# Kernel optimization log

Hardware: AMD Instinct MI355X
Metric: run time of the kernel (lower is better)

The kernel has to match this reference:

```python
import jax, jax.numpy as jnp
import numpy as np

# dims matching init_kwargs
B = 4096
NFIELD = 20
NFEAT = 100000
SQL_NEMB = 16
DATA_NEMB = 16
HID = 512
K = 16          # num_experts
C = 2           # select_experts (top-k)
OUT = 1
CARD = NFIELD + NFEAT + 1  # sql embedding rows
GATE_IN = NFIELD * SQL_NEMB   # 320
EXP_IN = NFIELD * DATA_NEMB   # 320
EPS = 1e-10


def _xavier(key, shape):
    fan_in, fan_out = shape[-2], shape[-1]
    a = np.sqrt(6.0 / (fan_in + fan_out)).astype(np.float32)
    return jax.random.uniform(key, shape, jnp.float32, -a, a)


def setup_inputs() -> dict:
    key = jax.random.key(0)
    ks = jax.random.split(key, 12)
    x = jax.random.randint(ks[0], (B, NFIELD), 0, NFEAT, dtype=jnp.int64)
    sql = jax.random.randint(ks[1], (B, NFIELD), 0, CARD, dtype=jnp.int64)
    return {
        "x": x,
        "sql": sql,
        "sql_emb_w": _xavier(ks[2], (CARD, SQL_NEMB)),
        "inp_emb_w": _xavier(ks[3], (NFEAT, DATA_NEMB)),
        # gate network: Linear(GATE_IN->HID) + relu + Linear(HID->K) + softmax
        "gw1": _xavier(ks[4], (GATE_IN, HID)),
        "gb1": jnp.zeros((HID,), jnp.float32),
        "gw2": _xavier(ks[5], (HID, K)),
        "gb2": jnp.zeros((K,), jnp.float32),
        # K expert DNNs: Linear(EXP_IN->HID) + relu + Linear(HID->OUT)
        "ew1": _xavier(ks[6], (K, EXP_IN, HID)),
        "eb1": jnp.zeros((K, HID), jnp.float32),
        "ew2": _xavier(ks[7], (K, HID, OUT)),
        "eb2": jnp.zeros((K, OUT), jnp.float32),
    }


def _cv_squared(v):
    # coefficient-of-variation squared, Shazeer-style load-balancing term
    return jnp.var(v) / (jnp.mean(v) ** 2 + EPS)


def reference(x, sql, sql_emb_w, inp_emb_w, gw1, gb1, gw2, gb2, ew1, eb1, ew2, eb2):
    b = x.shape[0]
    x_emb = inp_emb_w[x].reshape(b, -1)      # [B, NFIELD*DATA_NEMB]
    sql_emb = sql_emb_w[sql].reshape(b, -1)  # [B, NFIELD*SQL_NEMB]

    # gate network -> softmax scores over K experts
    h = jax.nn.relu(sql_emb @ gw1 + gb1)
    gate_scores = jax.nn.softmax(h @ gw2 + gb2, axis=-1)  # [B, K]

    # top-C sparse gating: keep top-C scores, renormalize, zero the rest
    top_v, top_i = jax.lax.top_k(gate_scores, C)
    top_v = top_v / jnp.sum(top_v, axis=-1, keepdims=True)
    gates = jnp.zeros((b, K), gate_scores.dtype).at[jnp.arange(b)[:, None], top_i].set(top_v)

    # expert MLPs (batched over expert dim; zero gates nullify unselected experts)
    eh = jax.nn.relu(jnp.einsum('bi,kih->bkh', x_emb, ew1) + eb1)   # [B, K, HID]
    eo = jnp.einsum('bkh,kho->bko', eh, ew2) + eb2                   # [B, K, OUT]
    y = jnp.sum(gates[:, :, None] * eo, axis=1).squeeze(-1)          # [B]

    importance = jnp.sum(gates, axis=0)                              # [K]
    load = jnp.sum((gates > 0).astype(gates.dtype), axis=0)         # [K]
    loss = _cv_squared(importance) + _cv_squared(load)
    return y, loss
```

## Files before the change

kernel.cpp:

```cpp
#include <hip/hip_runtime.h>

#define Bn 4096
#define NF 20
#define NEMB 16
#define HIDN 512
#define KE 16
#define GIN 320
#define NKS 10

typedef __attribute__((ext_vector_type(8))) short short8;
typedef __attribute__((ext_vector_type(4))) float f32x4;

__device__ __forceinline__ unsigned short f2bf(float f) {
  unsigned int u = __builtin_bit_cast(unsigned int, f);
  u += 0x7fff + ((u >> 16) & 1);
  return (unsigned short)(u >> 16);
}
__device__ __forceinline__ float bf2f(unsigned short h) {
  unsigned int u = ((unsigned int)h) << 16;
  return __builtin_bit_cast(float, u);
}

__device__ __forceinline__ void gload_lds16(const unsigned short* g, void* l) {
  __builtin_amdgcn_global_load_lds(
      (const __attribute__((address_space(1))) unsigned int*)g,
      (__attribute__((address_space(3))) unsigned int*)l, 16, 0, 0);
}

__device__ __forceinline__ void vwait(int n) {
  if (n >= 5) asm volatile("s_waitcnt vmcnt(5)" ::: "memory");
  else        asm volatile("s_waitcnt vmcnt(0)" ::: "memory");
  __builtin_amdgcn_sched_barrier(0);
}

__global__ __launch_bounds__(256) void prep_kernel(
    const int* __restrict__ sql, const float* __restrict__ semb,
    const float* __restrict__ gw1, const float* __restrict__ ew1,
    unsigned short* __restrict__ SH, unsigned short* __restrict__ SL,
    unsigned short* __restrict__ GWF, unsigned short* __restrict__ EWF,
    float* __restrict__ y, int* __restrict__ cnt) {
  long long t = (long long)blockIdx.x * 256 + threadIdx.x;
  if (t < 81920) {
    int row = (int)(t / NF), f = (int)(t % NF);
    int idx = sql[row * NF + f];
    const float4* s = (const float4*)(semb + (size_t)idx * NEMB);
    float4 v[4] = {s[0], s[1], s[2], s[3]};
    const float* sf = (const float*)v;
    short8 h0, h1, l0, l1;
#pragma unroll
    for (int i = 0; i < 8; i++) {
      float a = sf[i];
      unsigned short hb = f2bf(a);
      h0[i] = (short)hb; l0[i] = (short)f2bf(a - bf2f(hb));
      a = sf[8 + i];
      hb = f2bf(a);
      h1[i] = (short)hb; l1[i] = (short)f2bf(a - bf2f(hb));
    }
    size_t o = (size_t)row * GIN + f * NEMB;
    *(short8*)(SH + o) = h0; *(short8*)(SH + o + 8) = h1;
    *(short8*)(SL + o) = l0; *(short8*)(SL + o + 8) = l1;
    return;
  }
  t -= 81920;
  if (t < 40960) {
    int s = (int)(t / 20480), r = (int)(t % 20480);
    int ks = r / 2048, r2 = r % 2048, nt = r2 / 64, l = r2 % 64;
    int k0 = ks * 32 + (l >> 4) * 8, n = nt * 16 + (l & 15);
    short8 o;
#pragma unroll
    for (int j = 0; j < 8; j++) {
      float w = gw1[(size_t)(k0 + j) * HIDN + n];
      unsigned short hb = f2bf(w);
      o[j] = (s == 0) ? (short)hb : (short)f2bf(w - bf2f(hb));
    }
    *(short8*)(GWF + ((((size_t)s * NKS + ks) * 32 + nt) * 64 + l) * 8) = o;
    return;
  }
  t -= 40960;
  if (t < 327680) {
    int e = (int)(t / 20480), r = (int)(t % 20480);
    int ks = r / 2048, r2 = r % 2048, nt = r2 / 64, l = r2 % 64;
    int k0 = ks * 32 + (l >> 4) * 8, n = nt * 16 + (l & 15);
    const float* W = ew1 + (size_t)e * GIN * HIDN;
    short8 o;
#pragma unroll
    for (int j = 0; j < 8; j++) o[j] = (short)f2bf(W[(size_t)(k0 + j) * HIDN + n]);
    *(short8*)(EWF + ((((size_t)e * NKS + ks) * 32 + nt) * 64 + l) * 8) = o;
    return;
  }
  t -= 327680;
  if (t < Bn + 1) y[t] = 0.f;
  else if (t < Bn + 1 + KE) cnt[t - (Bn + 1)] = 0;
}

__global__ __launch_bounds__(256, 2) void gate_kernel(
    const unsigned short* __restrict__ SH, const unsigned short* __restrict__ SL,
    const unsigned short* __restrict__ GWF, const float* __restrict__ gb1,
    const float* __restrict__ gw2, float* __restrict__ glp) {
  __shared__ __align__(16) unsigned short ring[3][10240];
  __shared__ float hs[64][68];
  const int tid = threadIdx.x, lane = tid & 63, wv = tid >> 6;
  const int bid = blockIdx.x;
  const int xcd = bid & 7, r_ = bid >> 3;
  const int cb = r_ & 7;
  const int band = (8 * xcd + (r_ >> 3)) * 64;
  const int ntg = cb * 4 + wv;

  short8 bh[NKS], bl[NKS];
#pragma unroll
  for (int ks = 0; ks < NKS; ks++) {
    bh[ks] = *(const short8*)(GWF + ((size_t)(ks * 32 + ntg)) * 512 + lane * 8);
    bl[ks] = *(const short8*)(GWF + ((size_t)((NKS + ks) * 32 + ntg)) * 512 + lane * 8);
  }
  const int cl = wv * 16 + (lane & 15);
  const float b1v = gb1[cb * 64 + cl];
  __builtin_amdgcn_sched_barrier(0);

#define GSTG(pi, slot)                                                        \
  {                                                                           \
    _Pragma("unroll") for (int i = 0; i < 5; i++) {                           \
      int c = wv * 5 + i;                                                     \
      int hl = c >= 10, kss = c - hl * 10;                                    \
      const unsigned short* s_ = (hl ? SL : SH) +                             \
          (size_t)(band + (pi) * 16 + (lane & 15)) * GIN + kss * 32 +         \
          (lane >> 4) * 8;                                                    \
      gload_lds16(s_, &ring[slot][c * 512 + lane * 8]);                       \
    }                                                                         \
  }

  GSTG(0, 0) GSTG(1, 1)
  __builtin_amdgcn_sched_barrier(0);

#pragma unroll
  for (int p = 0; p < 4; p++) {
    vwait(p < 3 ? 5 : 0);
    __builtin_amdgcn_s_barrier();
    __builtin_amdgcn_sched_barrier(0);
    if (p + 2 < 4) GSTG(p + 2, (p + 2) % 3)
    __builtin_amdgcn_sched_barrier(0);
    const unsigned short* rb = ring[p % 3];
    f32x4 acc = {};
#pragma unroll
    for (int ks = 0; ks < NKS; ks++) {
      short8 ah = *(const short8*)&rb[ks * 512 + lane * 8];
      short8 al = *(const short8*)&rb[(NKS + ks) * 512 + lane * 8];
      acc = __builtin_amdgcn_mfma_f32_16x16x32_bf16(ah, bh[ks], acc, 0, 0, 0);
      acc = __builtin_amdgcn_mfma_f32_16x16x32_bf16(al, bh[ks], acc, 0, 0, 0);
      acc = __builtin_amdgcn_mfma_f32_16x16x32_bf16(ah, bl[ks], acc, 0, 0, 0);
    }
#pragma unroll
    for (int j = 0; j < 4; j++)
      hs[p * 16 + (lane >> 4) * 4 + j][cl] = fmaxf(acc[j] + b1v, 0.f);
  }
  __syncthreads();

  float (*g2s)[16] = (float(*)[16])&ring[0][0];
  ((float4*)g2s)[tid] = ((const float4*)(gw2 + (size_t)cb * 64 * KE))[tid];
  __syncthreads();
#pragma unroll
  for (int it = 0; it < 4; it++) {
    int row = it * 16 + (tid >> 4), q = tid & 15;
    float s = 0.f;
#pragma unroll 8
    for (int c = 0; c < 64; c++) s = fmaf(hs[row][c], g2s[c][q], s);
    glp[((size_t)cb * Bn + band + row) * KE + q] = s;
  }
#undef GSTG
}

__global__ __launch_bounds__(256) void gate2_kernel(
    const float* __restrict__ glp, const float* __restrict__ gb2,
    int* __restrict__ cnt, int* __restrict__ list, float* __restrict__ wlist) {
  __shared__ float part[4][64][KE];
  __shared__ int lcnt[KE];
  __shared__ int gbase[KE];
  const int tid = threadIdx.x;
  const int r = tid & 63, g = tid >> 6;
  const int row = blockIdx.x * 64 + r;
  if (tid < KE) lcnt[tid] = 0;
  float lg[KE];
#pragma unroll
  for (int q = 0; q < KE; q++) lg[q] = 0.f;
#pragma unroll
  for (int s2 = 0; s2 < 2; s2++) {
    const float4* a = (const float4*)(glp + ((size_t)(2 * g + s2) * Bn + row) * KE);
#pragma unroll
    for (int u = 0; u < 4; u++) {
      float4 v = a[u];
      lg[u * 4 + 0] += v.x; lg[u * 4 + 1] += v.y;
      lg[u * 4 + 2] += v.z; lg[u * 4 + 3] += v.w;
    }
  }
#pragma unroll
  for (int q = 0; q < KE; q++) part[g][r][q] = lg[q];
  __syncthreads();
  if (tid < 64) {
#pragma unroll
    for (int q = 0; q < KE; q++)
      lg[q] = part[0][tid][q] + part[1][tid][q] + part[2][tid][q] +
              part[3][tid][q] + gb2[q];
    float m = lg[0];
#pragma unroll
    for (int q = 1; q < KE; q++) m = fmaxf(m, lg[q]);
    float e[KE];
#pragma unroll
    for (int q = 0; q < KE; q++) e[q] = expf(lg[q] - m);
    int i1 = 0; float v1 = e[0];
#pragma unroll
    for (int q = 1; q < KE; q++) if (e[q] > v1) { v1 = e[q]; i1 = q; }
    int i2 = (i1 == 0) ? 1 : 0; float v2 = e[i2];
#pragma unroll
    for (int q = 0; q < KE; q++)
      if (q != i1 && e[q] > v2) { v2 = e[q]; i2 = q; }
    int rowg = blockIdx.x * 64 + tid;
    int o1 = atomicAdd(&lcnt[i1], 1);
    int o2 = atomicAdd(&lcnt[i2], 1);
    __syncthreads();
    if (tid < KE) gbase[tid] = atomicAdd(&cnt[tid], lcnt[tid]);
    __syncthreads();
    float den = v1 + v2;
    int s1 = gbase[i1] + o1;
    list[i1 * Bn + s1] = rowg; wlist[i1 * Bn + s1] = v1 / den;
    int s2 = gbase[i2] + o2;
    list[i2 * Bn + s2] = rowg; wlist[i2 * Bn + s2] = v2 / den;
  } else {
    __syncthreads();
    __syncthreads();
  }
}

__global__ __launch_bounds__(256) void packloss_kernel(
    const int* __restrict__ x, const float* __restrict__ demb,
    const int* __restrict__ cnt, const int* __restrict__ list,
    const float* __restrict__ wlist, unsigned short* __restrict__ XEP,
    float* __restrict__ out) {
  __shared__ float simp[KE][KE];
  __shared__ float fimp[KE];
  const int tid = threadIdx.x;
  const int bid = blockIdx.x;
  const int xcd = bid & 7, r_ = bid >> 3;
  const int k = xcd + 8 * (r_ & 1), jb = r_ >> 1;
  if (jb == 64) {
    if (k != 0) return;
    const int kk = tid >> 4, g = tid & 15;
    const int n = cnt[kk];
    float s = 0.f;
    for (int j = g; j < n; j += 16) s += wlist[kk * Bn + j];
    simp[kk][g] = s;
    __syncthreads();
    if (tid < KE) {
      float t = 0.f;
      for (int q = 0; q < KE; q++) t += simp[tid][q];
      fimp[tid] = t;
    }
    __syncthreads();
    if (tid == 0) {
      double mi = 0.0, ml = 0.0;
      for (int q = 0; q < KE; q++) { mi += fimp[q]; ml += (double)cnt[q]; }
      mi /= KE; ml /= KE;
      double vi = 0.0, vl = 0.0;
      for (int q = 0; q < KE; q++) {
        double di = fimp[q] - mi; vi += di * di;
        double dl = (double)cnt[q] - ml; vl += dl * dl;
      }
      vi /= KE; vl /= KE;
      out[Bn] = (float)(vi / (mi * mi + 1e-10) + vl / (ml * ml + 1e-10));
    }
    return;
  }
  const int n = cnt[k];
  if (jb * 64 >= n) return;
  unsigned short* reg = XEP + (size_t)k * 1310720;
#pragma unroll
  for (int it = 0; it < 5; it++) {
    int tt = it * 256 + tid;
    int i = jb * 64 + tt / NF, f = tt % NF;
    if (i < n) {
      int rid = list[k * Bn + i];
      int idx = x[rid * NF + f];
      const float4* s = (const float4*)(demb + (size_t)idx * NEMB);
      float4 v[4] = {s[0], s[1], s[2], s[3]};
      const float* sf = (const float*)v;
      short8 o0, o1;
#pragma unroll
      for (int e = 0; e < 8; e++) {
        o0[e] = (short)f2bf(sf[e]);
        o1[e] = (short)f2bf(sf[8 + e]);
      }
      int panel = i >> 5, mt = (i >> 4) & 1, lr = i & 15;
      int ks = f >> 1, ko0 = (f & 1) * 2;
      unsigned short* d =
          reg + (size_t)panel * 10240 + ks * 1024 + mt * 512 + ko0 * 128 + lr * 8;
      *(short8*)d = o0;
      *(short8*)(d + 128) = o1;
    }
  }
}

__global__ __launch_bounds__(256, 2) void expert_kernel(
    const unsigned short* __restrict__ XEP, const unsigned short* __restrict__ EWF,
    const float* __restrict__ eb1, const float* __restrict__ ew2,
    const float* __restrict__ eb2, const int* __restrict__ cnt,
    const int* __restrict__ list, const float* __restrict__ wlist,
    float* __restrict__ y) {
  __shared__ __align__(16) unsigned short ring[3][10240];
  __shared__ float pb[16][4][32];
  const int tid = threadIdx.x, lane = tid & 63, wv = tid >> 6;
  const int bid = blockIdx.x;
  const int xcd = bid & 7, r_ = bid >> 3;
  const int k = xcd + 8 * (r_ & 1);
  const int cb = (r_ >> 1) & 3, qz = r_ >> 3;
  const int n = cnt[k];
  const int np = (n + 31) >> 5;
  const int npb = (np > qz) ? ((np - qz + 7) >> 3) : 0;
  if (npb == 0) return;
  const unsigned short* XEPk = XEP + (size_t)k * 1310720;
  const int kBn = k * Bn;

  float b1v[2], w2v[2];
#pragma unroll
  for (int nt = 0; nt < 2; nt++) {
    int colg = cb * 128 + (wv * 2 + nt) * 16 + (lane & 15);
    b1v[nt] = eb1[(size_t)k * HIDN + colg];
    w2v[nt] = ew2[(size_t)k * HIDN + colg];
  }
  short8 bb[2][NKS];
#pragma unroll
  for (int nt = 0; nt < 2; nt++)
#pragma unroll
    for (int ks = 0; ks < NKS; ks++)
      bb[nt][ks] = *(const short8*)(
          EWF + ((size_t)((k * NKS + ks) * 32 + cb * 8 + wv * 2 + nt)) * 512 +
          lane * 8);
  __builtin_amdgcn_sched_barrier(0);

#define ESTG(pi, slot)                                                        \
  {                                                                           \
    _Pragma("unroll") for (int i = 0; i < 5; i++) {                           \
      int c = wv * 5 + i;                                                     \
      gload_lds16(XEPk + (size_t)(pi) * 10240 + c * 512 + lane * 8,           \
                  &ring[slot][c * 512 + lane * 8]);                           \
    }                                                                         \
  }

  ESTG(qz, 0)
  if (npb > 1) ESTG(qz + 8, 1)
  __builtin_amdgcn_sched_barrier(0);

  for (int p = 0; p < npb; p++) {
    vwait((p + 1 < npb) ? 5 : 0);
    __builtin_amdgcn_s_barrier();
    __builtin_amdgcn_sched_barrier(0);
    if (p + 2 < npb) ESTG(qz + 8 * (p + 2), (p + 2) % 3)
    __builtin_amdgcn_sched_barrier(0);
    const unsigned short* rb = ring[p % 3];
    f32x4 acc[2][2] = {};
#pragma unroll
    for (int ks = 0; ks < NKS; ks++) {
      short8 a0 = *(const short8*)&rb[ks * 1024 + lane * 8];
      short8 a1 = *(const short8*)&rb[ks * 1024 + 512 + lane * 8];
      acc[0][0] = __builtin_amdgcn_mfma_f32_16x16x32_bf16(a0, bb[0][ks], acc[0][0], 0, 0, 0);
      acc[0][1] = __builtin_amdgcn_mfma_f32_16x16x32_bf16(a0, bb[1][ks], acc[0][1], 0, 0, 0);
      acc[1][0] = __builtin_amdgcn_mfma_f32_16x16x32_bf16(a1, bb[0][ks], acc[1][0], 0, 0, 0);
      acc[1][1] = __builtin_amdgcn_mfma_f32_16x16x32_bf16(a1, bb[1][ks], acc[1][1], 0, 0, 0);
    }
    float part[2][4];
#pragma unroll
    for (int mt = 0; mt < 2; mt++)
#pragma unroll
      for (int j = 0; j < 4; j++)
        part[mt][j] = fmaxf(acc[mt][0][j] + b1v[0], 0.f) * w2v[0] +
                      fmaxf(acc[mt][1][j] + b1v[1], 0.f) * w2v[1];
#pragma unroll
    for (int off = 8; off >= 1; off >>= 1)
#pragma unroll
      for (int mt = 0; mt < 2; mt++)
#pragma unroll
        for (int j = 0; j < 4; j++)
          part[mt][j] += __shfl_xor(part[mt][j], off);
    if ((lane & 15) == 0) {
#pragma unroll
      for (int mt = 0; mt < 2; mt++)
#pragma unroll
        for (int j = 0; j < 4; j++)
          pb[p][wv][mt * 16 + (lane >> 4) * 4 + j] = part[mt][j];
    }
  }
  __syncthreads();

  const float e2 = (cb == 0) ? eb2[k] : 0.f;
  for (int t = tid; t < npb * 32; t += 256) {
    int pp = t >> 5, r = t & 31;
    int i = (qz + 8 * pp) * 32 + r;
    if (i < n) {
      float v = pb[pp][0][r] + pb[pp][1][r] + pb[pp][2][r] + pb[pp][3][r];
      atomicAdd(&y[list[kBn + i]], wlist[kBn + i] * (v + e2));
    }
  }
#undef ESTG
}

extern "C" void kernel_launch(void* const* d_in, const int* in_sizes, int n_in,
                              void* d_out, int out_size, void* d_ws, size_t ws_size,
                              hipStream_t stream) {
  const int* x      = (const int*)d_in[0];
  const int* sql    = (const int*)d_in[1];
  const float* semb = (const float*)d_in[2];
  const float* demb = (const float*)d_in[3];
  const float* gw1  = (const float*)d_in[4];
  const float* gb1  = (const float*)d_in[5];
  const float* gw2  = (const float*)d_in[6];
  const float* gb2  = (const float*)d_in[7];
  const float* ew1  = (const float*)d_in[8];
  const float* eb1  = (const float*)d_in[9];
  const float* ew2  = (const float*)d_in[10];
  const float* eb2  = (const float*)d_in[11];
  float* y = (float*)d_out;

  char* ws = (char*)d_ws;
  int* cnt            = (int*)(ws);
  int* list           = (int*)(ws + 4096);
  float* wlist        = (float*)(ws + 266240);
  float* glp          = (float*)(ws + 528384);
  unsigned short* SH  = (unsigned short*)(ws + 5246976);
  unsigned short* SL  = (unsigned short*)(ws + 7868416);
  unsigned short* GWF = (unsigned short*)(ws + 10489856);
  unsigned short* EWF = (unsigned short*)(ws + 11145216);
  unsigned short* XEP = (unsigned short*)(ws + 16777216);

  prep_kernel<<<1777, 256, 0, stream>>>(sql, semb, gw1, ew1,
                                        SH, SL, GWF, EWF, y, cnt);
  gate_kernel<<<512, 256, 0, stream>>>(SH, SL, GWF, gb1, gw2, glp);
  gate2_kernel<<<64, 256, 0, stream>>>(glp, gb2, cnt, list, wlist);
  packloss_kernel<<<1040, 256, 0, stream>>>(x, demb, cnt, list, wlist, XEP, y);
  expert_kernel<<<512, 256, 0, stream>>>(XEP, EWF, eb1, ew2, eb2,
                                         cnt, list, wlist, y);
}
```

Before: 72.81 us.

## Fuse embedding packing into gating kernel and move loss into expert kernel

The separate packloss kernel is removed. Each gate2 block now scatters the bf16-packed data embeddings for its own 64 rows straight to their assigned expert slots, using the top-2 choices it just computed. The loss computation moves into one extra block of the expert kernel. This saves a kernel launch and the re-read of list indirection, but the packing now runs on only 64 blocks, so there is less parallelism for the gather.

```diff
diff --git a/kernel.cpp b/kernel.cpp
--- a/kernel.cpp
+++ b/kernel.cpp
@@ -168,12 +168,16 @@
 #undef GSTG
 }
 
-__global__ __launch_bounds__(256) void gate2_kernel(
+__global__ __launch_bounds__(256) void gate2pack_kernel(
     const float* __restrict__ glp, const float* __restrict__ gb2,
-    int* __restrict__ cnt, int* __restrict__ list, float* __restrict__ wlist) {
+    const int* __restrict__ x, const float* __restrict__ demb,
+    int* __restrict__ cnt, int* __restrict__ list, float* __restrict__ wlist,
+    unsigned short* __restrict__ XEP) {
   __shared__ float part[4][64][KE];
   __shared__ int lcnt[KE];
   __shared__ int gbase[KE];
+  __shared__ int selk[64][2];
+  __shared__ int seli[64][2];
   const int tid = threadIdx.x;
   const int r = tid & 63, g = tid >> 6;
   const int row = blockIdx.x * 64 + r;
@@ -182,8 +186,8 @@
 #pragma unroll
   for (int q = 0; q < KE; q++) lg[q] = 0.f;
 #pragma unroll
-  for (int s2 = 0; s2 < 2; s2++) {
-    const float4* a = (const float4*)(glp + ((size_t)(2 * g + s2) * Bn + row) * KE);
+  for (int s2_ = 0; s2_ < 2; s2_++) {
+    const float4* a = (const float4*)(glp + ((size_t)(2 * g + s2_) * Bn + row) * KE);
 #pragma unroll
     for (int u = 0; u < 4; u++) {
       float4 v = a[u];
@@ -194,6 +198,9 @@
 #pragma unroll
   for (int q = 0; q < KE; q++) part[g][r][q] = lg[q];
   __syncthreads();
+
+  int i1 = 0, i2 = 0, o1 = 0, o2 = 0;
+  float v1 = 0.f, v2 = 0.f;
   if (tid < 64) {
 #pragma unroll
     for (int q = 0; q < KE; q++)
@@ -205,43 +212,71 @@
     float e[KE];
 #pragma unroll
     for (int q = 0; q < KE; q++) e[q] = expf(lg[q] - m);
-    int i1 = 0; float v1 = e[0];
+    v1 = e[0];
 #pragma unroll
     for (int q = 1; q < KE; q++) if (e[q] > v1) { v1 = e[q]; i1 = q; }
-    int i2 = (i1 == 0) ? 1 : 0; float v2 = e[i2];
+    i2 = (i1 == 0) ? 1 : 0; v2 = e[i2];
 #pragma unroll
     for (int q = 0; q < KE; q++)
       if (q != i1 && e[q] > v2) { v2 = e[q]; i2 = q; }
+    o1 = atomicAdd(&lcnt[i1], 1);
+    o2 = atomicAdd(&lcnt[i2], 1);
+  }
+  __syncthreads();
+  if (tid < KE) gbase[tid] = atomicAdd(&cnt[tid], lcnt[tid]);
+  __syncthreads();
+  if (tid < 64) {
     int rowg = blockIdx.x * 64 + tid;
-    int o1 = atomicAdd(&lcnt[i1], 1);
-    int o2 = atomicAdd(&lcnt[i2], 1);
-    __syncthreads();
-    if (tid < KE) gbase[tid] = atomicAdd(&cnt[tid], lcnt[tid]);
-    __syncthreads();
     float den = v1 + v2;
     int s1 = gbase[i1] + o1;
     list[i1 * Bn + s1] = rowg; wlist[i1 * Bn + s1] = v1 / den;
     int s2 = gbase[i2] + o2;
     list[i2 * Bn + s2] = rowg; wlist[i2 * Bn + s2] = v2 / den;
-  } else {
-    __syncthreads();
-    __syncthreads();
-  }
-}
-
-__global__ __launch_bounds__(256) void packloss_kernel(
-    const int* __restrict__ x, const float* __restrict__ demb,
-    const int* __restrict__ cnt, const int* __restrict__ list,
-    const float* __restrict__ wlist, unsigned short* __restrict__ XEP,
-    float* __restrict__ out) {
-  __shared__ float simp[KE][KE];
-  __shared__ float fimp[KE];
-  const int tid = threadIdx.x;
+    selk[tid][0] = i1; seli[tid][0] = s1;
+    selk[tid][1] = i2; seli[tid][1] = s2;
+  }
+  __syncthreads();
+
+#pragma unroll 2
+  for (int it = 0; it < 10; it++) {
+    int t = it * 256 + tid;
+    int entry = t / NF, f = t % NF;
+    int rr = entry >> 1, ch = entry & 1;
+    int k = selk[rr][ch], i = seli[rr][ch];
+    int rid = blockIdx.x * 64 + rr;
+    int idx = x[rid * NF + f];
+    const float4* s = (const float4*)(demb + (size_t)idx * NEMB);
+    float4 v[4] = {s[0], s[1], s[2], s[3]};
+    const float* sf = (const float*)v;
+    short8 q0, q1;
+#pragma unroll
+    for (int e = 0; e < 8; e++) {
+      q0[e] = (short)f2bf(sf[e]);
+      q1[e] = (short)f2bf(sf[8 + e]);
+    }
+    int panel = i >> 5, mt = (i >> 4) & 1, lr = i & 15;
+    int ks = f >> 1, ko0 = (f & 1) * 2;
+    unsigned short* d = XEP + (size_t)k * 1310720 + (size_t)panel * 10240 +
+                        ks * 1024 + mt * 512 + ko0 * 128 + lr * 8;
+    *(short8*)d = q0;
+    *(short8*)(d + 128) = q1;
+  }
+}
+
+__global__ __launch_bounds__(256, 2) void expert_kernel(
+    const unsigned short* __restrict__ XEP, const unsigned short* __restrict__ EWF,
+    const float* __restrict__ eb1, const float* __restrict__ ew2,
+    const float* __restrict__ eb2, const int* __restrict__ cnt,
+    const int* __restrict__ list, const float* __restrict__ wlist,
+    float* __restrict__ y) {
+  __shared__ __align__(16) unsigned short ring[3][10240];
+  __shared__ float pb[16][4][32];
+  const int tid = threadIdx.x, lane = tid & 63, wv = tid >> 6;
   const int bid = blockIdx.x;
-  const int xcd = bid & 7, r_ = bid >> 3;
-  const int k = xcd + 8 * (r_ & 1), jb = r_ >> 1;
-  if (jb == 64) {
-    if (k != 0) return;
+
+  if (bid == 512) {
+    float (*simp)[KE] = (float(*)[KE])&pb[0][0][0];
+    float* fimp = &pb[8][0][0];
     const int kk = tid >> 4, g = tid & 15;
     const int n = cnt[kk];
     float s = 0.f;
@@ -264,49 +299,11 @@
         double dl = (double)cnt[q] - ml; vl += dl * dl;
       }
       vi /= KE; vl /= KE;
-      out[Bn] = (float)(vi / (mi * mi + 1e-10) + vl / (ml * ml + 1e-10));
+      y[Bn] = (float)(vi / (mi * mi + 1e-10) + vl / (ml * ml + 1e-10));
     }
     return;
   }
-  const int n = cnt[k];
-  if (jb * 64 >= n) return;
-  unsigned short* reg = XEP + (size_t)k * 1310720;
-#pragma unroll
-  for (int it = 0; it < 5; it++) {
-    int tt = it * 256 + tid;
-    int i = jb * 64 + tt / NF, f = tt % NF;
-    if (i < n) {
-      int rid = list[k * Bn + i];
-      int idx = x[rid * NF + f];
-      const float4* s = (const float4*)(demb + (size_t)idx * NEMB);
-      float4 v[4] = {s[0], s[1], s[2], s[3]};
-      const float* sf = (const float*)v;
-      short8 o0, o1;
-#pragma unroll
-      for (int e = 0; e < 8; e++) {
-        o0[e] = (short)f2bf(sf[e]);
-        o1[e] = (short)f2bf(sf[8 + e]);
-      }
-      int panel = i >> 5, mt = (i >> 4) & 1, lr = i & 15;
-      int ks = f >> 1, ko0 = (f & 1) * 2;
-      unsigned short* d =
-          reg + (size_t)panel * 10240 + ks * 1024 + mt * 512 + ko0 * 128 + lr * 8;
-      *(short8*)d = o0;
-      *(short8*)(d + 128) = o1;
-    }
-  }
-}
-
-__global__ __launch_bounds__(256, 2) void expert_kernel(
-    const unsigned short* __restrict__ XEP, const unsigned short* __restrict__ EWF,
-    const float* __restrict__ eb1, const float* __restrict__ ew2,
-    const float* __restrict__ eb2, const int* __restrict__ cnt,
-    const int* __restrict__ list, const float* __restrict__ wlist,
-    float* __restrict__ y) {
-  __shared__ __align__(16) unsigned short ring[3][10240];
-  __shared__ float pb[16][4][32];
-  const int tid = threadIdx.x, lane = tid & 63, wv = tid >> 6;
-  const int bid = blockIdx.x;
+
   const int xcd = bid & 7, r_ = bid >> 3;
   const int k = xcd + 8 * (r_ & 1);
   const int cb = (r_ >> 1) & 3, qz = r_ >> 3;
@@ -431,8 +428,8 @@
   prep_kernel<<<1777, 256, 0, stream>>>(sql, semb, gw1, ew1,
                                         SH, SL, GWF, EWF, y, cnt);
   gate_kernel<<<512, 256, 0, stream>>>(SH, SL, GWF, gb1, gw2, glp);
-  gate2_kernel<<<64, 256, 0, stream>>>(glp, gb2, cnt, list, wlist);
-  packloss_kernel<<<1040, 256, 0, stream>>>(x, demb, cnt, list, wlist, XEP, y);
-  expert_kernel<<<512, 256, 0, stream>>>(XEP, EWF, eb1, ew2, eb2,
+  gate2pack_kernel<<<64, 256, 0, stream>>>(glp, gb2, x, demb,
+                                           cnt, list, wlist, XEP);
+  expert_kernel<<<513, 256, 0, stream>>>(XEP, EWF, eb1, ew2, eb2,
                                          cnt, list, wlist, y);
 }
```

New measurement: 63.44 us (median of 2 runs). -12.9%, faster.
